# Optimization experiments

Measured on AMD Instinct MI355X. Metric: run time of the kernel, lower is better.

Reference implementation:

```python
import jax, jax.numpy as jnp
import numpy as np

B, T, I, H, O = 64, 512, 128, 1024, 128
ALPHA = 0.2


def setup_inputs() -> dict:
    key = jax.random.key(0)
    ks = jax.random.split(key, 7)
    inv_sqrt_h = 1.0 / np.sqrt(H)
    return {
        "x": jax.random.normal(ks[0], (B, T, I), dtype=jnp.float32),
        "wi": jax.random.normal(ks[1], (I, H), dtype=jnp.float32) / np.sqrt(I),
        "wrec": jax.random.normal(ks[2], (H, H), dtype=jnp.float32) * inv_sqrt_h,
        "wout": jax.random.normal(ks[3], (H, O), dtype=jnp.float32) * inv_sqrt_h,
        "b": jax.random.normal(ks[4], (H, 1), dtype=jnp.float32) * 0.1,
        "g": jax.random.normal(ks[5], (H, 1), dtype=jnp.float32) * 0.5 + 1.0,
        "h0": jax.random.normal(ks[6], (H,), dtype=jnp.float32) * 0.1,
    }


def reference(x, wi, wrec, wout, b, g, h0):
    # Leaky tanh RNN: h_{t+1} = h_t + alpha*(-h_t + (g*r_t) @ wrec^T + x_t @ wi)
    #                 r_t = tanh(h_t + b); out_t = (g*r_t) @ wout
    gv = g[:, 0]  # (H,)
    bv = b[:, 0]  # (H,)
    batch = x.shape[0]

    r0 = jnp.tanh(h0 + bv)                     # (H,)
    out0 = (gv * r0) @ wout                    # (O,) broadcast over batch

    h_init = jnp.broadcast_to(h0, (batch, h0.shape[0]))
    r_init = jnp.broadcast_to(r0, (batch, h0.shape[0]))

    # precompute input projection for all steps used in the loop (steps 0..T-2)
    xs = jnp.swapaxes(x[:, :-1, :], 0, 1)      # (T-1, B, I)

    def step(carry, x_t):
        h, r = carry
        h = h + ALPHA * (-h + (gv * r) @ wrec.T + x_t @ wi)
        r = jnp.tanh(h + bv)
        out = (gv * r) @ wout                  # (B, O)
        return (h, r), out

    _, outs = jax.lax.scan(step, (h_init, r_init), xs)   # (T-1, B, O)
    outs = jnp.swapaxes(outs, 0, 1)                      # (B, T-1, O)
    out0b = jnp.broadcast_to(out0, (batch, 1, wout.shape[1]))
    return jnp.concatenate([out0b, outs], axis=1)        # (B, T, O)
```

## Files before the change

kernel.cpp:

```cpp
#include <hip/hip_runtime.h>

#define H 1024
#define I_DIM 128
#define O_DIM 128
#define T_DIM 512
#define ALPHA 0.2f
#define NWG 64
#define JSL 64

typedef short short8 __attribute__((ext_vector_type(8)));
typedef float f32x4 __attribute__((ext_vector_type(4)));

__device__ __forceinline__ unsigned short f2b(float f) {
    union { float f; unsigned u; } x; x.f = f;
    unsigned u = x.u;
    return (unsigned short)((u + 0x7FFFu + ((u >> 16) & 1u)) >> 16);
}
__device__ __forceinline__ float tanh_fast(float x) {
    float e = __expf(2.0f * x);
    return 1.0f - 2.0f * __builtin_amdgcn_rcpf(e + 1.0f);
}
__device__ __forceinline__ short8 ld8f(const float* __restrict__ p) {
    const float4 a = *(const float4*)p;
    const float4 b = *(const float4*)(p + 4);
    short8 r;
    r[0]=(short)f2b(a.x); r[1]=(short)f2b(a.y); r[2]=(short)f2b(a.z); r[3]=(short)f2b(a.w);
    r[4]=(short)f2b(b.x); r[5]=(short)f2b(b.y); r[6]=(short)f2b(b.z); r[7]=(short)f2b(b.w);
    return r;
}
__device__ __forceinline__ void async16(const unsigned short* g, unsigned short* l) {
    __builtin_amdgcn_global_load_lds(
        (const __attribute__((address_space(1))) unsigned int*)(const void*)g,
        (__attribute__((address_space(3))) unsigned int*)(void*)l, 16, 0, 0);
}

__global__ __launch_bounds__(256, 1) void rnn_kernel(
    const float* __restrict__ x, const float* __restrict__ wi,
    const float* __restrict__ wrec, const float* __restrict__ wout,
    const float* __restrict__ bb, const float* __restrict__ gg,
    const float* __restrict__ h0p, float* __restrict__ out,
    unsigned short* __restrict__ aG, unsigned int* __restrict__ bar)
{
    __shared__ unsigned short abuf[32 * 512];
    __shared__ unsigned short aloc[2 * 512];

    const int tid  = threadIdx.x;
    const int w    = tid >> 6, lane = tid & 63;
    const int n    = lane & 15, q = lane >> 4;
    const int grp  = blockIdx.x & 3;
    const int ji   = blockIdx.x >> 2;
    const int j0   = ji * JSL;
    const int j    = j0 + w * 16 + n;
    const int b0   = grp * 16;

    short8 wfr[32];
#pragma unroll
    for (int kt = 0; kt < 32; ++kt)
        wfr[kt] = ld8f(&wrec[(size_t)j * H + kt * 32 + q * 8]);

    short8 wifr[4];
#pragma unroll
    for (int kt = 0; kt < 4; ++kt) {
        short8 v;
#pragma unroll
        for (int i = 0; i < 8; ++i)
            v[i] = (short)f2b(wi[(size_t)(kt * 32 + q * 8 + i) * H + j]);
        wifr[kt] = v;
    }
    short8 wofr[2][2];
#pragma unroll
    for (int oti = 0; oti < 2; ++oti)
#pragma unroll
        for (int ktl = 0; ktl < 2; ++ktl) {
            short8 v; const int o = (2 * w + oti) * 16 + n;
#pragma unroll
            for (int i = 0; i < 8; ++i)
                v[i] = (short)f2b(wout[(size_t)(j0 + ktl * 32 + q * 8 + i) * O_DIM + o]);
            wofr[oti][ktl] = v;
        }

    const float gv = gg[j], bv = bb[j];
    const float h00 = h0p[j];
    float hreg[4];
#pragma unroll
    for (int r = 0; r < 4; ++r) hreg[r] = h00;

    const int off_g = (j >> 5) * 512 + ((j & 31) >> 3) * 128 + (j & 7);
    const int kl    = w * 16 + n;
    const int off_l = (kl >> 5) * 512 + ((kl & 31) >> 3) * 128 + (kl & 7);

    auto do_out = [&](int t) {
        short8 af0 = *(const short8*)&aloc[lane * 8];
        short8 af1 = *(const short8*)&aloc[512 + lane * 8];
        f32x4 o0 = {0.f,0.f,0.f,0.f}, o1 = {0.f,0.f,0.f,0.f};
        o0 = __builtin_amdgcn_mfma_f32_16x16x32_bf16(af0, wofr[0][0], o0, 0,0,0);
        o1 = __builtin_amdgcn_mfma_f32_16x16x32_bf16(af0, wofr[1][0], o1, 0,0,0);
        o0 = __builtin_amdgcn_mfma_f32_16x16x32_bf16(af1, wofr[0][1], o0, 0,0,0);
        o1 = __builtin_amdgcn_mfma_f32_16x16x32_bf16(af1, wofr[1][1], o1, 0,0,0);
#pragma unroll
        for (int r = 0; r < 4; ++r) {
            size_t row = ((size_t)(b0 + 4*q + r) * T_DIM + t) * O_DIM;
            atomicAdd(&out[row + (2*w + 0)*16 + n], o0[r]);
            atomicAdd(&out[row + (2*w + 1)*16 + n], o1[r]);
        }
    };

    {
        unsigned short a0 = f2b(gv * tanh_fast(h00 + bv));
        unsigned short* d0 = aG + (size_t)grp * 16384;
#pragma unroll
        for (int r = 0; r < 4; ++r) {
            d0[off_g + (4*q + r) * 8] = a0;
            aloc[off_l + (4*q + r) * 8] = a0;
        }
    }
    __syncthreads();
    if (tid == 0) __hip_atomic_fetch_add(bar, 1u, __ATOMIC_RELEASE, __HIP_MEMORY_SCOPE_AGENT);

    short8 xfr[4];
#pragma unroll
    for (int kt = 0; kt < 4; ++kt)
        xfr[kt] = ld8f(&x[(size_t)(b0 + n) * T_DIM * I_DIM + kt * 32 + q * 8]);

    do_out(0);

    for (int t = 1; t < T_DIM; ++t) {
        if (tid == 0) {
            const unsigned target = (unsigned)NWG * (unsigned)t;
            while (__hip_atomic_load(bar, __ATOMIC_ACQUIRE, __HIP_MEMORY_SCOPE_AGENT) < target)
                __builtin_amdgcn_s_sleep(1);
        }
        __syncthreads();

        const unsigned short* src = aG + ((size_t)((t - 1) & 1) * 4 + grp) * 16384;
#pragma unroll
        for (int c = 0; c < 8; ++c) {
            const int chunk = w * 8 + c;
            async16(src + chunk * 512 + lane * 8, abuf + chunk * 512);
        }
        __syncthreads();

        f32x4 acc0 = {0.f,0.f,0.f,0.f}, acc1 = {0.f,0.f,0.f,0.f};
        acc0 = __builtin_amdgcn_mfma_f32_16x16x32_bf16(xfr[0], wifr[0], acc0, 0,0,0);
        acc1 = __builtin_amdgcn_mfma_f32_16x16x32_bf16(xfr[1], wifr[1], acc1, 0,0,0);
        acc0 = __builtin_amdgcn_mfma_f32_16x16x32_bf16(xfr[2], wifr[2], acc0, 0,0,0);
        acc1 = __builtin_amdgcn_mfma_f32_16x16x32_bf16(xfr[3], wifr[3], acc1, 0,0,0);
#pragma unroll
        for (int kt = 0; kt < 32; kt += 2) {
            short8 a0f = *(const short8*)&abuf[kt * 512 + lane * 8];
            short8 a1f = *(const short8*)&abuf[(kt + 1) * 512 + lane * 8];
            acc0 = __builtin_amdgcn_mfma_f32_16x16x32_bf16(a0f, wfr[kt],     acc0, 0,0,0);
            acc1 = __builtin_amdgcn_mfma_f32_16x16x32_bf16(a1f, wfr[kt + 1], acc1, 0,0,0);
        }

        unsigned short* dst = aG + ((size_t)(t & 1) * 4 + grp) * 16384;
#pragma unroll
        for (int r = 0; r < 4; ++r) {
            float z  = acc0[r] + acc1[r];
            float hv = (1.0f - ALPHA) * hreg[r] + ALPHA * z;
            hreg[r] = hv;
            unsigned short ab = f2b(gv * tanh_fast(hv + bv));
            dst[off_g + (4*q + r) * 8] = ab;
            aloc[off_l + (4*q + r) * 8] = ab;
        }
        __syncthreads();
        if (tid == 0) __hip_atomic_fetch_add(bar, 1u, __ATOMIC_RELEASE, __HIP_MEMORY_SCOPE_AGENT);

        if (t < T_DIM - 1) {
#pragma unroll
            for (int kt = 0; kt < 4; ++kt)
                xfr[kt] = ld8f(&x[((size_t)(b0 + n) * T_DIM + t) * I_DIM + kt * 32 + q * 8]);
        }
        do_out(t);
    }
}

extern "C" void kernel_launch(void* const* d_in, const int* in_sizes, int n_in,
                              void* d_out, int out_size, void* d_ws, size_t ws_size,
                              hipStream_t stream) {
    const float* x    = (const float*)d_in[0];
    const float* wi   = (const float*)d_in[1];
    const float* wrec = (const float*)d_in[2];
    const float* wout = (const float*)d_in[3];
    const float* bb   = (const float*)d_in[4];
    const float* gg   = (const float*)d_in[5];
    const float* h0   = (const float*)d_in[6];
    float* outp = (float*)d_out;

    unsigned short* aG = (unsigned short*)d_ws;
    unsigned int* bar  = (unsigned int*)((char*)d_ws + 2 * 4 * 16384 * 2);

    hipMemsetAsync(d_out, 0, (size_t)64 * T_DIM * O_DIM * sizeof(float), stream);
    hipMemsetAsync(bar, 0, 64, stream);
    hipLaunchKernelGGL(rnn_kernel, dim3(NWG), dim3(256), 0, stream,
                       x, wi, wrec, wout, bb, gg, h0, outp, aG, bar);
}
```

Before: 2.181 ms.

## Use per-batch-group barriers and compute output from full activations without atomics

Each batch group of 16 workgroups now syncs on its own counter, padded 64 words apart, instead of one global barrier over all 64 workgroups. The input-projection MFMAs are issued before the barrier wait so they overlap with it. The output projection is redone: each workgroup computes an 8-column output slice from the full gathered activation buffer of the previous step, reduces it across waves in LDS, and writes it directly. This removes the float atomics and the memset of the output. Activation writes to global are coalesced through LDS as short8 stores, and the output lags one step behind, which adds extra syncthreads and an epilogue wait.

```diff
diff --git a/kernel.cpp b/kernel.cpp
--- a/kernel.cpp
+++ b/kernel.cpp
@@ -6,7 +6,7 @@
 #define T_DIM 512
 #define ALPHA 0.2f
 #define NWG 64
-#define JSL 64
+#define GSZ 16
 
 typedef short short8 __attribute__((ext_vector_type(8)));
 typedef float f32x4 __attribute__((ext_vector_type(4)));
@@ -42,16 +42,18 @@
     unsigned short* __restrict__ aG, unsigned int* __restrict__ bar)
 {
     __shared__ unsigned short abuf[32 * 512];
-    __shared__ unsigned short aloc[2 * 512];
+    __shared__ unsigned short aloc[1024];
+    __shared__ float opart[4 * 128];
 
     const int tid  = threadIdx.x;
     const int w    = tid >> 6, lane = tid & 63;
     const int n    = lane & 15, q = lane >> 4;
     const int grp  = blockIdx.x & 3;
     const int ji   = blockIdx.x >> 2;
-    const int j0   = ji * JSL;
+    const int j0   = ji * 64;
     const int j    = j0 + w * 16 + n;
     const int b0   = grp * 16;
+    unsigned int* gbar = bar + grp * 64;
 
     short8 wfr[32];
 #pragma unroll
@@ -67,84 +69,80 @@
             v[i] = (short)f2b(wi[(size_t)(kt * 32 + q * 8 + i) * H + j]);
         wifr[kt] = v;
     }
-    short8 wofr[2][2];
-#pragma unroll
-    for (int oti = 0; oti < 2; ++oti)
-#pragma unroll
-        for (int ktl = 0; ktl < 2; ++ktl) {
-            short8 v; const int o = (2 * w + oti) * 16 + n;
-#pragma unroll
-            for (int i = 0; i < 8; ++i)
-                v[i] = (short)f2b(wout[(size_t)(j0 + ktl * 32 + q * 8 + i) * O_DIM + o]);
-            wofr[oti][ktl] = v;
-        }
-
-    const float gv = gg[j], bv = bb[j];
-    const float h00 = h0p[j];
+    short8 wofr[8];
+#pragma unroll
+    for (int kk = 0; kk < 8; ++kk) {
+        short8 v;
+        const int kb = (w * 8 + kk) * 32 + q * 8;
+#pragma unroll
+        for (int i = 0; i < 8; ++i)
+            v[i] = (n < 8) ? (short)f2b(wout[(size_t)(kb + i) * O_DIM + ji * 8 + n]) : (short)0;
+        wofr[kk] = v;
+    }
+
+    const float gv = gg[j], bv = bb[j], h00 = h0p[j];
     float hreg[4];
 #pragma unroll
     for (int r = 0; r < 4; ++r) hreg[r] = h00;
 
-    const int off_g = (j >> 5) * 512 + ((j & 31) >> 3) * 128 + (j & 7);
     const int kl    = w * 16 + n;
     const int off_l = (kl >> 5) * 512 + ((kl & 31) >> 3) * 128 + (kl & 7);
 
     auto do_out = [&](int t) {
-        short8 af0 = *(const short8*)&aloc[lane * 8];
-        short8 af1 = *(const short8*)&aloc[512 + lane * 8];
-        f32x4 o0 = {0.f,0.f,0.f,0.f}, o1 = {0.f,0.f,0.f,0.f};
-        o0 = __builtin_amdgcn_mfma_f32_16x16x32_bf16(af0, wofr[0][0], o0, 0,0,0);
-        o1 = __builtin_amdgcn_mfma_f32_16x16x32_bf16(af0, wofr[1][0], o1, 0,0,0);
-        o0 = __builtin_amdgcn_mfma_f32_16x16x32_bf16(af1, wofr[0][1], o0, 0,0,0);
-        o1 = __builtin_amdgcn_mfma_f32_16x16x32_bf16(af1, wofr[1][1], o1, 0,0,0);
-#pragma unroll
-        for (int r = 0; r < 4; ++r) {
-            size_t row = ((size_t)(b0 + 4*q + r) * T_DIM + t) * O_DIM;
-            atomicAdd(&out[row + (2*w + 0)*16 + n], o0[r]);
-            atomicAdd(&out[row + (2*w + 1)*16 + n], o1[r]);
+        f32x4 oa = {0.f, 0.f, 0.f, 0.f};
+#pragma unroll
+        for (int kk = 0; kk < 8; ++kk) {
+            short8 af = *(const short8*)&abuf[(w * 8 + kk) * 512 + lane * 8];
+            oa = __builtin_amdgcn_mfma_f32_16x16x32_bf16(af, wofr[kk], oa, 0, 0, 0);
+        }
+        if (n < 8) {
+#pragma unroll
+            for (int r = 0; r < 4; ++r) opart[w * 128 + (4 * q + r) * 8 + n] = oa[r];
+        }
+        __syncthreads();
+        if (tid < 128) {
+            float s = opart[tid] + opart[128 + tid] + opart[256 + tid] + opart[384 + tid];
+            const int m = tid >> 3, c = tid & 7;
+            out[((size_t)(b0 + m) * T_DIM + t) * O_DIM + ji * 8 + c] = s;
         }
     };
 
     {
         unsigned short a0 = f2b(gv * tanh_fast(h00 + bv));
-        unsigned short* d0 = aG + (size_t)grp * 16384;
-#pragma unroll
-        for (int r = 0; r < 4; ++r) {
-            d0[off_g + (4*q + r) * 8] = a0;
-            aloc[off_l + (4*q + r) * 8] = a0;
-        }
+        unsigned short* d0 = aG + (size_t)grp * 16384 + ji * 1024;
+#pragma unroll
+        for (int r = 0; r < 4; ++r) d0[off_l + (4 * q + r) * 8] = a0;
     }
     __syncthreads();
-    if (tid == 0) __hip_atomic_fetch_add(bar, 1u, __ATOMIC_RELEASE, __HIP_MEMORY_SCOPE_AGENT);
+    if (tid == 0) __hip_atomic_fetch_add(gbar, 1u, __ATOMIC_RELEASE, __HIP_MEMORY_SCOPE_AGENT);
 
     short8 xfr[4];
 #pragma unroll
     for (int kt = 0; kt < 4; ++kt)
         xfr[kt] = ld8f(&x[(size_t)(b0 + n) * T_DIM * I_DIM + kt * 32 + q * 8]);
 
-    do_out(0);
-
     for (int t = 1; t < T_DIM; ++t) {
-        if (tid == 0) {
-            const unsigned target = (unsigned)NWG * (unsigned)t;
-            while (__hip_atomic_load(bar, __ATOMIC_ACQUIRE, __HIP_MEMORY_SCOPE_AGENT) < target)
-                __builtin_amdgcn_s_sleep(1);
-        }
-        __syncthreads();
-
-        const unsigned short* src = aG + ((size_t)((t - 1) & 1) * 4 + grp) * 16384;
-#pragma unroll
-        for (int c = 0; c < 8; ++c) {
-            const int chunk = w * 8 + c;
-            async16(src + chunk * 512 + lane * 8, abuf + chunk * 512);
-        }
-        __syncthreads();
-
         f32x4 acc0 = {0.f,0.f,0.f,0.f}, acc1 = {0.f,0.f,0.f,0.f};
         acc0 = __builtin_amdgcn_mfma_f32_16x16x32_bf16(xfr[0], wifr[0], acc0, 0,0,0);
         acc1 = __builtin_amdgcn_mfma_f32_16x16x32_bf16(xfr[1], wifr[1], acc1, 0,0,0);
         acc0 = __builtin_amdgcn_mfma_f32_16x16x32_bf16(xfr[2], wifr[2], acc0, 0,0,0);
         acc1 = __builtin_amdgcn_mfma_f32_16x16x32_bf16(xfr[3], wifr[3], acc1, 0,0,0);
+
+        if (tid == 0) {
+            const unsigned target = (unsigned)GSZ * (unsigned)t;
+            while (__hip_atomic_load(gbar, __ATOMIC_ACQUIRE, __HIP_MEMORY_SCOPE_AGENT) < target)
+                __builtin_amdgcn_s_sleep(1);
+        }
+        __syncthreads();
+
+        const unsigned short* src = aG + ((size_t)((t - 1) & 1) * 4 + grp) * 16384;
+#pragma unroll
+        for (int c = 0; c < 8; ++c) {
+            const int chunk = w * 8 + c;
+            async16(src + chunk * 512 + lane * 8, abuf + chunk * 512);
+        }
+        __syncthreads();
+
 #pragma unroll
         for (int kt = 0; kt < 32; kt += 2) {
             short8 a0f = *(const short8*)&abuf[kt * 512 + lane * 8];
@@ -153,26 +151,43 @@
             acc1 = __builtin_amdgcn_mfma_f32_16x16x32_bf16(a1f, wfr[kt + 1], acc1, 0,0,0);
         }
 
-        unsigned short* dst = aG + ((size_t)(t & 1) * 4 + grp) * 16384;
 #pragma unroll
         for (int r = 0; r < 4; ++r) {
             float z  = acc0[r] + acc1[r];
             float hv = (1.0f - ALPHA) * hreg[r] + ALPHA * z;
             hreg[r] = hv;
-            unsigned short ab = f2b(gv * tanh_fast(hv + bv));
-            dst[off_g + (4*q + r) * 8] = ab;
-            aloc[off_l + (4*q + r) * 8] = ab;
-        }
-        __syncthreads();
-        if (tid == 0) __hip_atomic_fetch_add(bar, 1u, __ATOMIC_RELEASE, __HIP_MEMORY_SCOPE_AGENT);
+            aloc[off_l + (4 * q + r) * 8] = f2b(gv * tanh_fast(hv + bv));
+        }
+        __syncthreads();
+
+        unsigned short* dst = aG + ((size_t)(t & 1) * 4 + grp) * 16384 + ji * 1024;
+        if (tid < 128) *(short8*)(dst + tid * 8) = *(const short8*)&aloc[tid * 8];
+        __syncthreads();
+        if (tid == 0) __hip_atomic_fetch_add(gbar, 1u, __ATOMIC_RELEASE, __HIP_MEMORY_SCOPE_AGENT);
+
+        do_out(t - 1);
 
         if (t < T_DIM - 1) {
 #pragma unroll
             for (int kt = 0; kt < 4; ++kt)
                 xfr[kt] = ld8f(&x[((size_t)(b0 + n) * T_DIM + t) * I_DIM + kt * 32 + q * 8]);
         }
-        do_out(t);
-    }
+    }
+
+    if (tid == 0) {
+        const unsigned target = (unsigned)GSZ * (unsigned)T_DIM;
+        while (__hip_atomic_load(gbar, __ATOMIC_ACQUIRE, __HIP_MEMORY_SCOPE_AGENT) < target)
+            __builtin_amdgcn_s_sleep(1);
+    }
+    __syncthreads();
+    const unsigned short* src = aG + ((size_t)((T_DIM - 1) & 1) * 4 + grp) * 16384;
+#pragma unroll
+    for (int c = 0; c < 8; ++c) {
+        const int chunk = w * 8 + c;
+        async16(src + chunk * 512 + lane * 8, abuf + chunk * 512);
+    }
+    __syncthreads();
+    do_out(T_DIM - 1);
 }
 
 extern "C" void kernel_launch(void* const* d_in, const int* in_sizes, int n_in,
@@ -190,8 +205,7 @@
     unsigned short* aG = (unsigned short*)d_ws;
     unsigned int* bar  = (unsigned int*)((char*)d_ws + 2 * 4 * 16384 * 2);
 
-    hipMemsetAsync(d_out, 0, (size_t)64 * T_DIM * O_DIM * sizeof(float), stream);
-    hipMemsetAsync(bar, 0, 64, stream);
+    hipMemsetAsync(bar, 0, 1024, stream);
     hipLaunchKernelGGL(rnn_kernel, dim3(NWG), dim3(256), 0, stream,
                        x, wi, wrec, wout, bb, gg, h0, outp, aG, bar);
 }
```

New measurement: 2.121 ms. -2.8%, faster.
